# Kernel optimization log

Hardware: AMD Instinct MI355X
Metric: run time of the kernel (lower is better)

Reference implementation:

```python
import jax, jax.numpy as jnp
import numpy as np

NEG_SLOPE = 0.01  # nn.LeakyReLU default


def setup_inputs() -> dict:
    key = jax.random.key(0)
    k1, k2, k3, k4, k5 = jax.random.split(key, 5)
    SLI, FEAT, NODE = 8, 64, 20000
    N = SLI * NODE          # 160000 graph nodes
    E = 2_560_000           # avg degree 16
    OUT = 64
    inputs = jax.random.normal(k1, (SLI, FEAT, NODE), dtype=jnp.float32)
    src = jax.random.randint(k2, (E,), 0, N, dtype=jnp.int64)
    dst = jax.random.randint(k3, (E,), 0, N, dtype=jnp.int64)
    # GraphConv params (glorot-ish scale)
    W = jax.random.normal(k4, (FEAT, OUT), dtype=jnp.float32) / np.sqrt(FEAT)
    b = jnp.zeros((OUT,), dtype=jnp.float32)
    return {"inputs": inputs, "W": W, "b": b, "src": src, "dst": dst}


def reference(inputs, W, b, src, dst):
    # inputs: [sli, feat, node] -> [sli*node, feat]  (dropout is eval-mode identity)
    sli, feat, node = inputs.shape
    x = jnp.transpose(inputs, (0, 2, 1)).reshape(-1, feat)
    N = sli * node
    ones = jnp.ones(src.shape, dtype=x.dtype)
    deg_out = jax.ops.segment_sum(ones, src, num_segments=N)  # out-degree of src
    deg_in = jax.ops.segment_sum(ones, dst, num_segments=N)   # in-degree of dst
    norm_src = jnp.where(deg_out > 0, deg_out, 1.0) ** -0.5
    norm_dst = jnp.where(deg_in > 0, deg_in, 1.0) ** -0.5
    # norm='both': scale src feats, sum-aggregate over edges, scale dst
    h = x * norm_src[:, None]
    agg = jax.ops.segment_sum(h[src], dst, num_segments=N)    # [N, feat]
    agg = agg * norm_dst[:, None]
    out = agg @ W + b                                          # [N, out]
    out = jax.nn.leaky_relu(out, NEG_SLOPE)
    # [N, out] -> [sli, node, out] -> [sli, out, node]
    return jnp.transpose(out.reshape(sli, node, -1), (0, 2, 1))
```

## Files before the change

kernel.cpp:

```cpp
#include <hip/hip_runtime.h>
#include <hip/hip_bf16.h>

constexpr int SLI  = 8;
constexpr int FEAT = 64;
constexpr int NODE = 20000;
constexpr int NTOT = SLI * NODE;
constexpr int OUTF = 64;
constexpr int CAP  = 48;
constexpr int NBD  = 625;
constexpr int NBS  = 313;
constexpr int BCAPD = 4608;
constexpr int BCAPS = 8960;
constexpr int EPB  = 4096;
constexpr int NDST = NTOT / 256;
constexpr int NTB  = 313 * SLI;

typedef __attribute__((ext_vector_type(8))) short bf16x8;
typedef __attribute__((ext_vector_type(4))) float f32x4;

static __device__ inline unsigned short f2bf(float x) {
    unsigned u = __float_as_uint(x);
    unsigned r = (u + 0x7fffu + ((u >> 16) & 1u)) >> 16;
    return (unsigned short)r;
}

__global__ __launch_bounds__(512) void k_part(const int* __restrict__ src,
                                              const int* __restrict__ dst,
                                              int* __restrict__ cursor_d,
                                              unsigned* __restrict__ bucket_d,
                                              int* __restrict__ cursor_s,
                                              unsigned short* __restrict__ bucket_s, int E) {
    __shared__ unsigned       svalD[EPB];
    __shared__ unsigned short sbktD[EPB];
    __shared__ unsigned sS[EPB];
    __shared__ int histD[NBD], lcurD[NBD], baseD[NBD];
    __shared__ int histS[NBS], lcurS[NBS], baseS[NBS];
    __shared__ int goffD[64], goffS[64];
    int t  = threadIdx.x;
    int e0 = blockIdx.x * EPB;
    for (int i = t; i < NBD; i += 512) histD[i] = 0;
    for (int i = t; i < NBS; i += 512) histS[i] = 0;
    __syncthreads();
    int myS[8], myD[8];
#pragma unroll
    for (int i = 0; i < 2; ++i) {
        int j  = (e0 >> 2) + i * 512 + t;
        int b4 = j << 2;
        if (b4 + 3 < E) {
            int4 vs = ((const int4*)src)[j];
            int4 vd = ((const int4*)dst)[j];
            myS[4*i+0] = vs.x; myS[4*i+1] = vs.y; myS[4*i+2] = vs.z; myS[4*i+3] = vs.w;
            myD[4*i+0] = vd.x; myD[4*i+1] = vd.y; myD[4*i+2] = vd.z; myD[4*i+3] = vd.w;
        } else {
#pragma unroll
            for (int c = 0; c < 4; ++c) {
                int idx = b4 + c;
                myS[4*i+c] = (idx < E) ? src[idx] : -1;
                myD[4*i+c] = (idx < E) ? dst[idx] : -1;
            }
        }
    }
#pragma unroll
    for (int i = 0; i < 8; ++i) {
        if (myD[i] >= 0) {
            atomicAdd(&histD[myD[i] >> 8], 1);
            atomicAdd(&histS[myS[i] >> 9], 1);
        }
    }
    __syncthreads();
    int rbD[2], rbS0;
#pragma unroll
    for (int i = 0; i < 2; ++i) {
        int bb = t + i * 512;
        rbD[i] = (bb < NBD) ? atomicAdd(&cursor_d[bb], histD[bb]) : 0;
    }
    rbS0 = (t < NBS) ? atomicAdd(&cursor_s[t], histS[t]) : 0;
    int wv = t >> 6, ln = t & 63;
    if (wv == 0) {
        int b0 = ln * 10, s = 0;
#pragma unroll
        for (int j = 0; j < 10; ++j) { int bb = b0 + j; if (bb < NBD) s += histD[bb]; }
        int x = s;
        for (int off = 1; off < 64; off <<= 1) {
            int y = __shfl_up(x, off, 64);
            if (ln >= off) x += y;
        }
        goffD[ln] = x - s;
    } else if (wv == 1) {
        int b0 = ln * 5, s = 0;
#pragma unroll
        for (int j = 0; j < 5; ++j) { int bb = b0 + j; if (bb < NBS) s += histS[bb]; }
        int x = s;
        for (int off = 1; off < 64; off <<= 1) {
            int y = __shfl_up(x, off, 64);
            if (ln >= off) x += y;
        }
        goffS[ln] = x - s;
    }
    asm volatile("s_waitcnt lgkmcnt(0)\n\ts_barrier" ::: "memory");
    for (int bb = t; bb < NBD; bb += 512) {
        int g = bb / 10;
        int sD = goffD[g];
        for (int k = g * 10; k < bb; ++k) sD += histD[k];
        lcurD[bb] = sD;
    }
    for (int bb = t; bb < NBS; bb += 512) {
        int g = bb / 5;
        int sS2 = goffS[g];
        for (int k = g * 5; k < bb; ++k) sS2 += histS[k];
        lcurS[bb] = sS2;
    }
    asm volatile("s_waitcnt lgkmcnt(0)\n\ts_barrier" ::: "memory");
#pragma unroll
    for (int i = 0; i < 8; ++i) {
        if (myD[i] >= 0) {
            int bD = myD[i] >> 8;
            int p  = atomicAdd(&lcurD[bD], 1);
            svalD[p] = ((unsigned)(myD[i] & 255) << 18) | (unsigned)myS[i];
            sbktD[p] = (unsigned short)bD;
            int bS = myS[i] >> 9;
            int q  = atomicAdd(&lcurS[bS], 1);
            sS[q] = ((unsigned)bS << 9) | (unsigned)(myS[i] & 511);
        }
    }
#pragma unroll
    for (int i = 0; i < 2; ++i) { int bb = t + i * 512; if (bb < NBD) baseD[bb] = rbD[i]; }
    if (t < NBS) baseS[t] = rbS0;
    __syncthreads();
    int nval = E - e0; if (nval > EPB) nval = EPB;
    for (int p = t; p < nval; p += 512) {
        int bD = sbktD[p];
        int wi = baseD[bD] + (p - (lcurD[bD] - histD[bD]));
        if (wi < BCAPD) bucket_d[(size_t)bD * BCAPD + wi] = svalD[p];
        unsigned vs = sS[p];
        int bS = vs >> 9;
        int wj = baseS[bS] + (p - (lcurS[bS] - histS[bS]));
        if (wj < BCAPS) bucket_s[(size_t)bS * BCAPS + wj] = (unsigned short)(vs & 511);
    }
}

__global__ __launch_bounds__(512) void k_finS(const int* __restrict__ cursor_s,
                                              const unsigned short* __restrict__ bucket_s,
                                              int* __restrict__ deg_out) {
    __shared__ int cnt[512];
    int t = threadIdx.x, b = blockIdx.x;
    cnt[t] = 0;
    __syncthreads();
    int len = cursor_s[b]; if (len > BCAPS) len = BCAPS;
    const unsigned short* p = bucket_s + (size_t)b * BCAPS;
    for (int i = t; i < len; i += 512)
        atomicAdd(&cnt[p[i]], 1);
    __syncthreads();
    int n0 = b << 9;
    if (n0 + t < NTOT) deg_out[n0 + t] = cnt[t];
}

__global__ __launch_bounds__(512) void k_fin2(const int* __restrict__ cursor_d,
                                              const unsigned* __restrict__ bucket_d,
                                              int* __restrict__ col_ell,
                                              int* __restrict__ deg_in,
                                              const float* __restrict__ in,
                                              const int* __restrict__ deg_out,
                                              unsigned short* __restrict__ xs) {
    __shared__ char lds[256 * CAP * 4 + 2048];
    int t = threadIdx.x;
    if (blockIdx.x < NDST) {
        int* ell = (int*)lds;
        int* cnt = (int*)(lds + 256 * CAP * 4);
        int b = blockIdx.x;
        if (t < 256) cnt[t] = 0;
        __syncthreads();
        int len = cursor_d[b]; if (len > BCAPD) len = BCAPD;
        const unsigned* p = bucket_d + (size_t)b * BCAPD;
        for (int i = t; i < len; i += 512) {
            unsigned e = p[i];
            int r = (e >> 18) & 255;
            int pos = atomicAdd(&cnt[r], 1);
            if (pos < CAP) ell[r * CAP + pos] = (int)(e & 0x3FFFFu);
        }
        __syncthreads();
        int node0 = b << 8;
        if (t < 256) deg_in[node0 + t] = cnt[t];
        size_t gbase = (size_t)node0 * CAP;
        const int4* lsrc = (const int4*)ell;
        int4* gdst = (int4*)(col_ell + gbase);
#pragma unroll
        for (int i = 0; i < 6; ++i)
            gdst[i * 512 + t] = lsrc[i * 512 + t];
    } else {
        float (*tile)[65] = (float(*)[65])lds;
        int tb  = blockIdx.x - NDST;
        int sli = tb / 313, nblk = tb - sli * 313;
        int n0  = nblk * 64;
        const float* ip = in + (size_t)sli * FEAT * NODE;
        int fx = t & 15;
        int fr = t >> 4;
        int nq = n0 + fx * 4;
#pragma unroll
        for (int i = 0; i < 2; ++i) {
            int f = fr + i * 32;
            float4 v = {0.f, 0.f, 0.f, 0.f};
            if (nq < NODE) v = *(const float4*)(ip + (size_t)f * NODE + nq);
            tile[f][fx * 4 + 0] = v.x;
            tile[f][fx * 4 + 1] = v.y;
            tile[f][fx * 4 + 2] = v.z;
            tile[f][fx * 4 + 3] = v.w;
        }
        __syncthreads();
        int h  = t & 31;
        int nr = t >> 5;
#pragma unroll
        for (int i = 0; i < 4; ++i) {
            int nl   = nr + i * 16;
            int node = n0 + nl;
            if (node < NODE) {
                int n = sli * NODE + node;
                int d = deg_out[n];
                float sc = rsqrtf(d > 0 ? (float)d : 1.f);
                unsigned lo = f2bf(tile[2 * h][nl] * sc);
                unsigned hi = f2bf(tile[2 * h + 1][nl] * sc);
                *(unsigned*)(xs + (size_t)n * 64 + 2 * h) = lo | (hi << 16);
            }
        }
    }
}

__global__ __launch_bounds__(256) void k_agg_gemm(const int* __restrict__ deg_in,
                                                  const int* __restrict__ col_ell,
                                                  const unsigned short* __restrict__ xs,
                                                  const float* __restrict__ W,
                                                  const float* __restrict__ b,
                                                  float* __restrict__ out) {
    __shared__ char lds[18432];
    unsigned short* av = (unsigned short*)lds;
    unsigned short* wt = (unsigned short*)(lds + 9216);
    float (*otile)[65] = (float(*)[65])lds;

    int t    = threadIdx.x;
    int lane = t & 63;
    int w    = t >> 6;
    int g8   = lane >> 3;
    int f8   = lane & 7;
    int sli  = blockIdx.y;
    int n0   = blockIdx.x * 64;

#pragma unroll
    for (int i = 0; i < 16; ++i) {
        int idx = i * 256 + t;
        int f = idx >> 6, o = idx & 63;
        wt[o * 72 + f] = f2bf(W[idx]);
    }

    int m0 = w * 16;
    for (int ii = 0; ii < 16; ii += 2) {
        int rowA = m0 + ii, rowB = rowA + 1;
        int nodeA = n0 + rowA, nodeB = n0 + rowB;
        int nA = sli * NODE + nodeA, nB = sli * NODE + nodeB;
        int dA = (nodeA < NODE) ? deg_in[nA] : 0;
        int dB = (nodeB < NODE) ? deg_in[nB] : 0;
        int degA = dA < CAP ? dA : CAP;
        int degB = dB < CAP ? dB : CAP;
        int cA = (lane < degA) ? col_ell[(size_t)nA * CAP + lane] : NTOT;
        int cB = (lane < degB) ? col_ell[(size_t)nB * CAP + lane] : NTOT;
        float accA[8] = {0,0,0,0,0,0,0,0};
        float accB[8] = {0,0,0,0,0,0,0,0};
        int gmax = degA > degB ? degA : degB;
        int groups = (gmax + 7) >> 3;
#pragma unroll 2
        for (int j = 0; j < groups; ++j) {
            int idx = 8 * j + g8;
            int sA = __shfl(cA, idx, 64);
            int sB = __shfl(cB, idx, 64);
            uint4 vA = *(const uint4*)(xs + (size_t)sA * 64 + f8 * 8);
            uint4 vB = *(const uint4*)(xs + (size_t)sB * 64 + f8 * 8);
            accA[0] += __uint_as_float(vA.x << 16);
            accA[1] += __uint_as_float(vA.x & 0xffff0000u);
            accA[2] += __uint_as_float(vA.y << 16);
            accA[3] += __uint_as_float(vA.y & 0xffff0000u);
            accA[4] += __uint_as_float(vA.z << 16);
            accA[5] += __uint_as_float(vA.z & 0xffff0000u);
            accA[6] += __uint_as_float(vA.w << 16);
            accA[7] += __uint_as_float(vA.w & 0xffff0000u);
            accB[0] += __uint_as_float(vB.x << 16);
            accB[1] += __uint_as_float(vB.x & 0xffff0000u);
            accB[2] += __uint_as_float(vB.y << 16);
            accB[3] += __uint_as_float(vB.y & 0xffff0000u);
            accB[4] += __uint_as_float(vB.z << 16);
            accB[5] += __uint_as_float(vB.z & 0xffff0000u);
            accB[6] += __uint_as_float(vB.w << 16);
            accB[7] += __uint_as_float(vB.w & 0xffff0000u);
        }
#pragma unroll
        for (int k = 0; k < 8; ++k) {
            accA[k] += __shfl_xor(accA[k], 8, 64);
            accA[k] += __shfl_xor(accA[k], 16, 64);
            accA[k] += __shfl_xor(accA[k], 32, 64);
            accB[k] += __shfl_xor(accB[k], 8, 64);
            accB[k] += __shfl_xor(accB[k], 16, 64);
            accB[k] += __shfl_xor(accB[k], 32, 64);
        }
        if (g8 == 0) {
            float scA = rsqrtf(dA > 0 ? (float)dA : 1.f);
            float scB = rsqrtf(dB > 0 ? (float)dB : 1.f);
            uint4 hv;
            hv.x = (unsigned)f2bf(accA[0] * scA) | ((unsigned)f2bf(accA[1] * scA) << 16);
            hv.y = (unsigned)f2bf(accA[2] * scA) | ((unsigned)f2bf(accA[3] * scA) << 16);
            hv.z = (unsigned)f2bf(accA[4] * scA) | ((unsigned)f2bf(accA[5] * scA) << 16);
            hv.w = (unsigned)f2bf(accA[6] * scA) | ((unsigned)f2bf(accA[7] * scA) << 16);
            ((uint4*)(av + rowA * 72))[f8] = hv;
            hv.x = (unsigned)f2bf(accB[0] * scB) | ((unsigned)f2bf(accB[1] * scB) << 16);
            hv.y = (unsigned)f2bf(accB[2] * scB) | ((unsigned)f2bf(accB[3] * scB) << 16);
            hv.z = (unsigned)f2bf(accB[4] * scB) | ((unsigned)f2bf(accB[5] * scB) << 16);
            hv.w = (unsigned)f2bf(accB[6] * scB) | ((unsigned)f2bf(accB[7] * scB) << 16);
            ((uint4*)(av + rowB * 72))[f8] = hv;
        }
    }

    __syncthreads();

    int q = lane >> 4, r16 = lane & 15;
    bf16x8 afr[2], bfr[4][2];
#pragma unroll
    for (int ks = 0; ks < 2; ++ks)
        afr[ks] = *(const bf16x8*)(av + (m0 + r16) * 72 + ks * 32 + q * 8);
#pragma unroll
    for (int nt = 0; nt < 4; ++nt)
#pragma unroll
        for (int ks = 0; ks < 2; ++ks)
            bfr[nt][ks] = *(const bf16x8*)(wt + (nt * 16 + r16) * 72 + ks * 32 + q * 8);

    f32x4 acc4[4];
#pragma unroll
    for (int nt = 0; nt < 4; ++nt) acc4[nt] = (f32x4){0.f, 0.f, 0.f, 0.f};
#pragma unroll
    for (int nt = 0; nt < 4; ++nt)
#pragma unroll
        for (int ks = 0; ks < 2; ++ks)
            acc4[nt] = __builtin_amdgcn_mfma_f32_16x16x32_bf16(afr[ks], bfr[nt][ks], acc4[nt], 0, 0, 0);
    __syncthreads();

#pragma unroll
    for (int nt = 0; nt < 4; ++nt) {
        int oc = nt * 16 + r16;
        float bias = b[oc];
#pragma unroll
        for (int r = 0; r < 4; ++r) {
            float v = acc4[nt][r] + bias;
            v = v > 0.f ? v : 0.01f * v;
            otile[oc][m0 + q * 4 + r] = v;
        }
    }
    __syncthreads();

    const size_t obase = (size_t)sli * OUTF * NODE;
#pragma unroll
    for (int i = 0; i < 16; ++i) {
        int o    = w + i * 4;
        int node = n0 + lane;
        if (node < NODE)
            out[obase + (size_t)o * NODE + node] = otile[o][lane];
    }
}

extern "C" void kernel_launch(void* const* d_in, const int* in_sizes, int n_in,
                              void* d_out, int out_size, void* d_ws, size_t ws_size,
                              hipStream_t stream) {
    const float* inputs = (const float*)d_in[0];
    const float* W      = (const float*)d_in[1];
    const float* b      = (const float*)d_in[2];
    const int*   src    = (const int*)d_in[3];
    const int*   dst    = (const int*)d_in[4];
    float*       out    = (float*)d_out;
    const int E = in_sizes[3];

    char* ws = (char*)d_ws;
    const size_t szXs    = (size_t)(NTOT + 1) * 64 * 2;
    const size_t szDeg   = (size_t)NTOT * 4;
    const size_t szEll   = (size_t)NTOT * CAP * 4;
    const size_t szBd    = (size_t)NBD * BCAPD * 4;
    const size_t szBs    = (size_t)NBS * BCAPS * 2;

    unsigned short* xs       = (unsigned short*)ws;
    int*            deg_in   = (int*)(ws + szXs);
    int*            deg_out  = (int*)(ws + szXs + szDeg);
    int*            col_ell  = (int*)(ws + szXs + 2 * szDeg);
    unsigned*       bucket_d = (unsigned*)(ws + szXs + 2 * szDeg + szEll);
    unsigned short* bucket_s = (unsigned short*)(ws + szXs + 2 * szDeg + szEll + szBd);
    int*            cursors  = (int*)(ws + szXs + 2 * szDeg + szEll + szBd + szBs);
    int* cursor_d = cursors;
    int* cursor_s = cursors + NBD;

    hipMemsetAsync(cursors, 0, (size_t)(NBD + NBS) * 4, stream);
    hipMemsetAsync(xs + (size_t)NTOT * 64, 0, 64 * sizeof(unsigned short), stream);

    int PB = (E + EPB - 1) / EPB;
    k_part<<<PB, 512, 0, stream>>>(src, dst, cursor_d, bucket_d, cursor_s, bucket_s, E);

    k_finS<<<NBS, 512, 0, stream>>>(cursor_s, bucket_s, deg_out);

    k_fin2<<<NDST + NTB, 512, 0, stream>>>(cursor_d, bucket_d, col_ell, deg_in,
                                           inputs, deg_out, xs);

    dim3 tgrid((NODE + 63) / 64, SLI);
    k_agg_gemm<<<tgrid, 256, 0, stream>>>(deg_in, col_ell, xs, W, b, out);
}
```

Measured before the change: 222.4 us.

## Build per-tile ELL adjacency in LDS inside aggregation kernel, drop global col_ell

Removes the separate pass that turned destination buckets into a global ELL array and deg_in. Each aggregation block now scans the one or two 256-node destination buckets covering its 64 rows and builds a local ELL list and counts in LDS. This avoids writing and re-reading a large global col_ell array, at the cost of reading each bucket from two to four blocks, doing LDS atomics in the GEMM kernel, and using more LDS per block. The bucket capacity is also raised slightly.

```diff
diff --git a/kernel.cpp b/kernel.cpp
--- a/kernel.cpp
+++ b/kernel.cpp
@@ -9,10 +9,9 @@
 constexpr int CAP  = 48;
 constexpr int NBD  = 625;
 constexpr int NBS  = 313;
-constexpr int BCAPD = 4608;
+constexpr int BCAPD = 4864;
 constexpr int BCAPS = 8960;
 constexpr int EPB  = 4096;
-constexpr int NDST = NTOT / 256;
 constexpr int NTB  = 313 * SLI;
 
 typedef __attribute__((ext_vector_type(8))) short bf16x8;
@@ -155,86 +154,58 @@
     if (n0 + t < NTOT) deg_out[n0 + t] = cnt[t];
 }
 
-__global__ __launch_bounds__(512) void k_fin2(const int* __restrict__ cursor_d,
-                                              const unsigned* __restrict__ bucket_d,
-                                              int* __restrict__ col_ell,
-                                              int* __restrict__ deg_in,
-                                              const float* __restrict__ in,
+__global__ __launch_bounds__(512) void k_tran(const float* __restrict__ in,
                                               const int* __restrict__ deg_out,
                                               unsigned short* __restrict__ xs) {
-    __shared__ char lds[256 * CAP * 4 + 2048];
-    int t = threadIdx.x;
-    if (blockIdx.x < NDST) {
-        int* ell = (int*)lds;
-        int* cnt = (int*)(lds + 256 * CAP * 4);
-        int b = blockIdx.x;
-        if (t < 256) cnt[t] = 0;
-        __syncthreads();
-        int len = cursor_d[b]; if (len > BCAPD) len = BCAPD;
-        const unsigned* p = bucket_d + (size_t)b * BCAPD;
-        for (int i = t; i < len; i += 512) {
-            unsigned e = p[i];
-            int r = (e >> 18) & 255;
-            int pos = atomicAdd(&cnt[r], 1);
-            if (pos < CAP) ell[r * CAP + pos] = (int)(e & 0x3FFFFu);
-        }
-        __syncthreads();
-        int node0 = b << 8;
-        if (t < 256) deg_in[node0 + t] = cnt[t];
-        size_t gbase = (size_t)node0 * CAP;
-        const int4* lsrc = (const int4*)ell;
-        int4* gdst = (int4*)(col_ell + gbase);
-#pragma unroll
-        for (int i = 0; i < 6; ++i)
-            gdst[i * 512 + t] = lsrc[i * 512 + t];
-    } else {
-        float (*tile)[65] = (float(*)[65])lds;
-        int tb  = blockIdx.x - NDST;
-        int sli = tb / 313, nblk = tb - sli * 313;
-        int n0  = nblk * 64;
-        const float* ip = in + (size_t)sli * FEAT * NODE;
-        int fx = t & 15;
-        int fr = t >> 4;
-        int nq = n0 + fx * 4;
-#pragma unroll
-        for (int i = 0; i < 2; ++i) {
-            int f = fr + i * 32;
-            float4 v = {0.f, 0.f, 0.f, 0.f};
-            if (nq < NODE) v = *(const float4*)(ip + (size_t)f * NODE + nq);
-            tile[f][fx * 4 + 0] = v.x;
-            tile[f][fx * 4 + 1] = v.y;
-            tile[f][fx * 4 + 2] = v.z;
-            tile[f][fx * 4 + 3] = v.w;
-        }
-        __syncthreads();
-        int h  = t & 31;
-        int nr = t >> 5;
-#pragma unroll
-        for (int i = 0; i < 4; ++i) {
-            int nl   = nr + i * 16;
-            int node = n0 + nl;
-            if (node < NODE) {
-                int n = sli * NODE + node;
-                int d = deg_out[n];
-                float sc = rsqrtf(d > 0 ? (float)d : 1.f);
-                unsigned lo = f2bf(tile[2 * h][nl] * sc);
-                unsigned hi = f2bf(tile[2 * h + 1][nl] * sc);
-                *(unsigned*)(xs + (size_t)n * 64 + 2 * h) = lo | (hi << 16);
-            }
-        }
-    }
-}
-
-__global__ __launch_bounds__(256) void k_agg_gemm(const int* __restrict__ deg_in,
-                                                  const int* __restrict__ col_ell,
+    __shared__ float tile[64][65];
+    int t   = threadIdx.x;
+    int tb  = blockIdx.x;
+    int sli = tb / 313, nblk = tb - sli * 313;
+    int n0  = nblk * 64;
+    const float* ip = in + (size_t)sli * FEAT * NODE;
+    int fx = t & 15;
+    int fr = t >> 4;
+    int nq = n0 + fx * 4;
+#pragma unroll
+    for (int i = 0; i < 2; ++i) {
+        int f = fr + i * 32;
+        float4 v = {0.f, 0.f, 0.f, 0.f};
+        if (nq < NODE) v = *(const float4*)(ip + (size_t)f * NODE + nq);
+        tile[f][fx * 4 + 0] = v.x;
+        tile[f][fx * 4 + 1] = v.y;
+        tile[f][fx * 4 + 2] = v.z;
+        tile[f][fx * 4 + 3] = v.w;
+    }
+    __syncthreads();
+    int h  = t & 31;
+    int nr = t >> 5;
+#pragma unroll
+    for (int i = 0; i < 4; ++i) {
+        int nl   = nr + i * 16;
+        int node = n0 + nl;
+        if (node < NODE) {
+            int n = sli * NODE + node;
+            int d = deg_out[n];
+            float sc = rsqrtf(d > 0 ? (float)d : 1.f);
+            unsigned lo = f2bf(tile[2 * h][nl] * sc);
+            unsigned hi = f2bf(tile[2 * h + 1][nl] * sc);
+            *(unsigned*)(xs + (size_t)n * 64 + 2 * h) = lo | (hi << 16);
+        }
+    }
+}
+
+__global__ __launch_bounds__(256) void k_agg_gemm(const int* __restrict__ cursor_d,
+                                                  const unsigned* __restrict__ bucket_d,
                                                   const unsigned short* __restrict__ xs,
                                                   const float* __restrict__ W,
                                                   const float* __restrict__ b,
                                                   float* __restrict__ out) {
-    __shared__ char lds[18432];
-    unsigned short* av = (unsigned short*)lds;
-    unsigned short* wt = (unsigned short*)(lds + 9216);
-    float (*otile)[65] = (float(*)[65])lds;
+    __shared__ char lds[30976];
+    int*            ell = (int*)lds;
+    int*            cnt = (int*)(lds + 12288);
+    unsigned short* av  = (unsigned short*)(lds + 12544);
+    unsigned short* wt  = (unsigned short*)(lds + 21760);
+    float (*otile)[65]  = (float(*)[65])lds;
 
     int t    = threadIdx.x;
     int lane = t & 63;
@@ -250,18 +221,38 @@
         int f = idx >> 6, o = idx & 63;
         wt[o * 72 + f] = f2bf(W[idx]);
     }
+    if (t < 64) cnt[t] = 0;
+    __syncthreads();
+
+    int g0 = sli * NODE + n0;
+    int b0 = g0 >> 8;
+    int b1 = (g0 + 63) >> 8;
+    if (b1 > (NTOT - 1) >> 8) b1 = (NTOT - 1) >> 8;
+    for (int bb = b0; bb <= b1; ++bb) {
+        int len = cursor_d[bb]; if (len > BCAPD) len = BCAPD;
+        const unsigned* p = bucket_d + (size_t)bb * BCAPD;
+        int gb = bb << 8;
+        for (int i = t; i < len; i += 256) {
+            unsigned e = p[i];
+            int row = gb + (int)(e >> 18) - g0;
+            if (row >= 0 && row < 64 && (n0 + row) < NODE) {
+                int pos = atomicAdd(&cnt[row], 1);
+                if (pos < CAP) ell[row * CAP + pos] = (int)(e & 0x3FFFFu);
+            }
+        }
+    }
+    __syncthreads();
 
     int m0 = w * 16;
     for (int ii = 0; ii < 16; ii += 2) {
         int rowA = m0 + ii, rowB = rowA + 1;
         int nodeA = n0 + rowA, nodeB = n0 + rowB;
-        int nA = sli * NODE + nodeA, nB = sli * NODE + nodeB;
-        int dA = (nodeA < NODE) ? deg_in[nA] : 0;
-        int dB = (nodeB < NODE) ? deg_in[nB] : 0;
+        int dA = (nodeA < NODE) ? cnt[rowA] : 0;
+        int dB = (nodeB < NODE) ? cnt[rowB] : 0;
         int degA = dA < CAP ? dA : CAP;
         int degB = dB < CAP ? dB : CAP;
-        int cA = (lane < degA) ? col_ell[(size_t)nA * CAP + lane] : NTOT;
-        int cB = (lane < degB) ? col_ell[(size_t)nB * CAP + lane] : NTOT;
+        int cA = (lane < degA) ? ell[rowA * CAP + lane] : NTOT;
+        int cB = (lane < degB) ? ell[rowB * CAP + lane] : NTOT;
         float accA[8] = {0,0,0,0,0,0,0,0};
         float accB[8] = {0,0,0,0,0,0,0,0};
         int gmax = degA > degB ? degA : degB;
@@ -374,19 +365,16 @@
     const int E = in_sizes[3];
 
     char* ws = (char*)d_ws;
-    const size_t szXs    = (size_t)(NTOT + 1) * 64 * 2;
-    const size_t szDeg   = (size_t)NTOT * 4;
-    const size_t szEll   = (size_t)NTOT * CAP * 4;
-    const size_t szBd    = (size_t)NBD * BCAPD * 4;
-    const size_t szBs    = (size_t)NBS * BCAPS * 2;
+    const size_t szXs  = (size_t)(NTOT + 1) * 64 * 2;
+    const size_t szDeg = (size_t)NTOT * 4;
+    const size_t szBd  = (size_t)NBD * BCAPD * 4;
+    const size_t szBs  = (size_t)NBS * BCAPS * 2;
 
     unsigned short* xs       = (unsigned short*)ws;
-    int*            deg_in   = (int*)(ws + szXs);
-    int*            deg_out  = (int*)(ws + szXs + szDeg);
-    int*            col_ell  = (int*)(ws + szXs + 2 * szDeg);
-    unsigned*       bucket_d = (unsigned*)(ws + szXs + 2 * szDeg + szEll);
-    unsigned short* bucket_s = (unsigned short*)(ws + szXs + 2 * szDeg + szEll + szBd);
-    int*            cursors  = (int*)(ws + szXs + 2 * szDeg + szEll + szBd + szBs);
+    int*            deg_out  = (int*)(ws + szXs);
+    unsigned*       bucket_d = (unsigned*)(ws + szXs + szDeg);
+    unsigned short* bucket_s = (unsigned short*)(ws + szXs + szDeg + szBd);
+    int*            cursors  = (int*)(ws + szXs + szDeg + szBd + szBs);
     int* cursor_d = cursors;
     int* cursor_s = cursors + NBD;
 
@@ -398,9 +386,8 @@
 
     k_finS<<<NBS, 512, 0, stream>>>(cursor_s, bucket_s, deg_out);
 
-    k_fin2<<<NDST + NTB, 512, 0, stream>>>(cursor_d, bucket_d, col_ell, deg_in,
-                                           inputs, deg_out, xs);
+    k_tran<<<NTB, 512, 0, stream>>>(inputs, deg_out, xs);
 
     dim3 tgrid((NODE + 63) / 64, SLI);
-    k_agg_gemm<<<tgrid, 256, 0, stream>>>(deg_in, col_ell, xs, W, b, out);
-}
+    k_agg_gemm<<<tgrid, 256, 0, stream>>>(cursor_d, bucket_d, xs, W, b, out);
+}
```

Result: slower. 229.2 us (+3.1%).
